# Kernel tuning notes

Measured on AMD Instinct MI355X. Metric: run time of the kernel, lower is better.

The kernel has to match this reference:

```python
import jax, jax.numpy as jnp
import numpy as np

B, N, H = 32, 2048, 256          # batch, num_docs, hidden_dim
F_HEADS = 8                      # config.dynamic_fusion_heads
NH = 8                           # num_heads inside each nn.MultiheadAttention
STEPS = 3                        # config.meta_adaptation_steps


def setup_inputs() -> dict:
    key = jax.random.key(0)
    ks = jax.random.split(key, 10)
    s = 0.02
    return {
        "query": jax.random.normal(ks[0], (B, H), jnp.float32),
        "retrieved_docs": jax.random.normal(ks[1], (B, N, H), jnp.float32),
        "causal_weights": jax.random.uniform(ks[2], (B, N, 1), jnp.float32),
        "context_history": jax.random.normal(ks[3], (B, H), jnp.float32),
        # per-fusion-head MultiheadAttention params (torch layout: in_proj [3H,H])
        "in_proj_w": jax.random.normal(ks[4], (F_HEADS, 3 * H, H), jnp.float32) * s,
        "in_proj_b": jnp.zeros((F_HEADS, 3 * H), jnp.float32),
        "out_proj_w": jax.random.normal(ks[5], (F_HEADS, H, H), jnp.float32) * s,
        "out_proj_b": jnp.zeros((F_HEADS, H), jnp.float32),
        "strategy_w": jax.random.normal(ks[6], (F_HEADS, H), jnp.float32) * s,
        "strategy_b": jnp.zeros((F_HEADS,), jnp.float32),
        "meta_params": jax.random.normal(ks[7], (STEPS, H, H), jnp.float32) * 0.02,
    }


def _mha_qlen1(q, kv, Wi, bi, Wo, bo):
    # q: [B,H] (query length 1), kv: [B,N,H]. Torch MHA semantics, batch_first.
    Wq, Wk, Wv = jnp.split(Wi, 3, axis=0)
    bq, bk, bv = jnp.split(bi, 3)
    dh = H // NH
    qh = (q @ Wq.T + bq).reshape(B, NH, dh)
    kh = (kv @ Wk.T + bk).reshape(B, N, NH, dh)
    vh = (kv @ Wv.T + bv).reshape(B, N, NH, dh)
    scores = jnp.einsum('bhd,bnhd->bhn', qh, kh) / jnp.sqrt(jnp.float32(dh))
    attn = jax.nn.softmax(scores, axis=-1)
    ctx = jnp.einsum('bhn,bnhd->bhd', attn, vh).reshape(B, H)
    return ctx @ Wo.T + bo


def reference(query, retrieved_docs, causal_weights, context_history,
              in_proj_w, in_proj_b, out_proj_w, out_proj_b,
              strategy_w, strategy_b, meta_params):
    # causal weighting of retrieved docs (shared across all fusion heads)
    weighted_docs = retrieved_docs * causal_weights  # [B,N,H]

    # batch all 8 fusion heads' cross-attention in one vmapped pass -> [F,B,H]
    heads_out = jax.vmap(
        lambda Wi, bi, Wo, bo: _mha_qlen1(query, weighted_docs, Wi, bi, Wo, bo)
    )(in_proj_w, in_proj_b, out_proj_w, out_proj_b)

    # sequential residual meta-adaptation steps (same matrices for every head)
    for i in range(STEPS):
        heads_out = heads_out + heads_out @ meta_params[i]

    # strategy-weighted combine of fusion heads
    strategy = jax.nn.softmax(query @ strategy_w.T + strategy_b, axis=-1)  # [B,F]
    return jnp.einsum('fbh,bf->bh', heads_out, strategy)  # [B,H]
```

## Files before the change

kernel.cpp:

```cpp
#include <hip/hip_runtime.h>
#include <hip/hip_bf16.h>


#define B_ 32
#define N_ 2048
#define H_ 256
#define F_ 8
#define FH_ 64
#define NCH_ 8
#define NCHK_ 4

typedef unsigned short u16;
typedef __attribute__((ext_vector_type(8))) short bf16x8;
typedef __attribute__((ext_vector_type(4))) float f32x4;
#define MFMA(a, b, c) __builtin_amdgcn_mfma_f32_16x16x32_bf16((a), (b), (c), 0, 0, 0)

__device__ __forceinline__ u16 f2b(float x) {
  unsigned u = __builtin_bit_cast(unsigned, x);
  return (u16)((u + 0x7fffu + ((u >> 16) & 1u)) >> 16);
}
__device__ __forceinline__ float b2f(u16 h) {
  unsigned u = ((unsigned)h) << 16;
  return __builtin_bit_cast(float, u);
}
__device__ __forceinline__ bf16x8 ld8b(const float* p) {
  float4 v0 = *(const float4*)p, v1 = *(const float4*)(p + 4);
  bf16x8 a;
  a[0] = f2b(v0.x); a[1] = f2b(v0.y); a[2] = f2b(v0.z); a[3] = f2b(v0.w);
  a[4] = f2b(v1.x); a[5] = f2b(v1.y); a[6] = f2b(v1.z); a[7] = f2b(v1.w);
  return a;
}

static constexpr size_t UB_U     = 0;
static constexpr size_t UB_W     = 1048576;
static constexpr size_t UB_L     = 3145728;
static constexpr size_t UB_STRAT = 3153920;
static constexpr size_t UB_MT    = 3154944;

#define SMEM_BYTES 52224

__device__ __forceinline__ void dev_k1(char* smem, int f, int hf, int bh,
    const float* __restrict__ query, const float* __restrict__ ipw,
    const float* __restrict__ ipb, const float* __restrict__ stw,
    const float* __restrict__ stb, u16* __restrict__ u, float* __restrict__ strat)
{
  const int tid = threadIdx.x, L = tid & 63, w = tid >> 6;
  const int khi = L >> 4, col = L & 15;
  u16* sW2 = (u16*)smem;
  u16* qhh = (u16*)(smem + 36864);
  u16* qhl = (u16*)(smem + 41216);
  float* slog = (float*)(smem + 45568);

  const int bg = bh * 16 + col;

  bf16x8 qf[8];
  #pragma unroll
  for (int ks = 0; ks < 8; ++ks)
    qf[ks] = ld8b(&query[(size_t)bg * H_ + ks * 32 + khi * 8]);

  if (f == 0 && hf == 0 && w == 0) {
    f32x4 sacc = (f32x4){0.f, 0.f, 0.f, 0.f};
    #pragma unroll
    for (int ks = 0; ks < 8; ++ks) {
      bf16x8 a = (bf16x8){0,0,0,0,0,0,0,0};
      if (col < 8) a = ld8b(&stw[(size_t)col * H_ + ks * 32 + khi * 8]);
      sacc = MFMA(a, qf[ks], sacc);
    }
    if (khi < 2) {
      #pragma unroll
      for (int r = 0; r < 4; ++r) {
        int i = khi * 4 + r;
        slog[col * 8 + i] = sacc[r] + stb[i];
      }
    }
  }

  bf16x8 aq[8];
  #pragma unroll
  for (int ks = 0; ks < 8; ++ks)
    aq[ks] = ld8b(&ipw[((size_t)(f * 768) + hf * 128 + w * 16 + col) * H_ + ks * 32 + khi * 8]);
  f32x4 qacc = (f32x4){0.f, 0.f, 0.f, 0.f};
  #pragma unroll
  for (int ks = 0; ks < 8; ++ks)
    qacc = MFMA(aq[ks], qf[ks], qacc);
  {
    int r0 = w * 16 + khi * 4;
    float4 bq = *(const float4*)&ipb[f * 768 + hf * 128 + r0];
    float v0 = qacc[0] + bq.x, v1 = qacc[1] + bq.y;
    float v2 = qacc[2] + bq.z, v3 = qacc[3] + bq.w;
    ushort4 hs = make_ushort4(f2b(v0), f2b(v1), f2b(v2), f2b(v3));
    ushort4 ls = make_ushort4(f2b(v0 - b2f(hs.x)), f2b(v1 - b2f(hs.y)),
                              f2b(v2 - b2f(hs.z)), f2b(v3 - b2f(hs.w)));
    *(ushort4*)&qhh[col * 136 + r0] = hs;
    *(ushort4*)&qhl[col * 136 + r0] = ls;
  }
  __syncthreads();

  if (f == 0 && hf == 0 && tid < 16) {
    float mx = slog[tid * 8];
    #pragma unroll
    for (int i = 1; i < F_; ++i) mx = fmaxf(mx, slog[tid * 8 + i]);
    float s = 0.f, e[F_];
    #pragma unroll
    for (int i = 0; i < F_; ++i) { e[i] = __expf(slog[tid * 8 + i] - mx); s += e[i]; }
    #pragma unroll
    for (int i = 0; i < F_; ++i) strat[(bh * 16 + tid) * F_ + i] = e[i] / s;
  }

  const float scale = 0.17677669529663687f;
  #pragma unroll
  for (int hp = 0; hp < 2; ++hp) {
    #pragma unroll
    for (int p = 0; p < 8; ++p) {
      int gid = tid + 512 * p;
      int dr = gid >> 6, jq = (gid & 63) * 4;
      float4 v = *(const float4*)&ipw[((size_t)(f * 768 + 256) + hf * 128 + hp * 64 + dr) * H_ + jq];
      float vv[4] = {v.x, v.y, v.z, v.w};
      #pragma unroll
      for (int e2 = 0; e2 < 4; ++e2) {
        int j = jq + e2;
        int m = ((((j >> 4) & 3) ^ ((j >> 2) & 3)) << 3);
        sW2[j * 72 + (dr ^ m)] = f2b(vv[e2]);
      }
    }
    __syncthreads();
    #pragma unroll
    for (int e = 0; e < 2; ++e) {
      #pragma unroll
      for (int q = 0; q < 2; ++q) {
        int jt = w * 2 + q;
        bf16x8 a = *(const bf16x8*)&sW2[(jt * 16 + col) * 72 + e * 32
                                        + ((khi ^ (jt & 3) ^ (col >> 2)) << 3)];
        int rl = (hp * 2 + e) * 32 + khi * 8;
        bf16x8 bhf = *(const bf16x8*)&qhh[col * 136 + rl];
        bf16x8 blf = *(const bf16x8*)&qhl[col * 136 + rl];
        f32x4 acc = (f32x4){0.f, 0.f, 0.f, 0.f};
        acc = MFMA(a, bhf, acc);
        acc = MFMA(a, blf, acc);
        int j0 = jt * 16 + khi * 4;
        ushort4 us = make_ushort4(f2b(acc[0] * scale), f2b(acc[1] * scale),
                                  f2b(acc[2] * scale), f2b(acc[3] * scale));
        *(ushort4*)&u[((size_t)(bg * 64) + f * 8 + hf * 4 + hp * 2 + e) * H_ + j0] = us;
      }
    }
    __syncthreads();
  }
}

__device__ __forceinline__ void dev_meta(char* smem, int bid2,
    const float* __restrict__ meta, u16* __restrict__ metaT)
{
  const int tid = threadIdx.x;
  const int s = bid2 >> 3, x0 = (bid2 & 7) * 32;
  u16* sT = (u16*)smem;
  #pragma unroll
  for (int p = 0; p < 4; ++p) {
    int idx = tid + 512 * p;
    int r = idx >> 3, xq = (idx & 7) * 4;
    float4 v = *(const float4*)&meta[((size_t)(s * 256) + r) * 256 + x0 + xq];
    sT[(xq + 0) * 264 + r] = f2b(v.x);
    sT[(xq + 1) * 264 + r] = f2b(v.y);
    sT[(xq + 2) * 264 + r] = f2b(v.z);
    sT[(xq + 3) * 264 + r] = f2b(v.w);
  }
  __syncthreads();
  #pragma unroll
  for (int p = 0; p < 2; ++p) {
    int idx = tid + 512 * p;
    int x = idx >> 5, rq = (idx & 31) * 8;
    bf16x8 v = *(bf16x8*)&sT[x * 264 + rq];
    *(bf16x8*)&metaT[((size_t)(s * 256) + x0 + x) * 256 + rq] = v;
  }
}

__device__ __forceinline__ void dev_k4(char* smem, int ns, int b,
    const float* __restrict__ docs, const float* __restrict__ cw,
    const u16* __restrict__ u, float* __restrict__ wbuf, float* __restrict__ lbuf)
{
  const int n0 = ns * 256;
  const int tid = threadIdx.x, L = tid & 63, w = tid >> 6;
  const int khi = L >> 4, col = L & 15;
  const int ft = w & 3, nt0 = (w >> 2) * 2;

  u16* sdu  = (u16*)smem;
  u16* phu  = (u16*)(smem + 33792);
  u16* plou = (u16*)(smem + 43008);

  bf16x8 uf[8];
  #pragma unroll
  for (int ks = 0; ks < 8; ++ks)
    uf[ks] = *(const bf16x8*)&u[((size_t)(b * 64) + ft * 16 + col) * H_ + ks * 32 + khi * 8];

  float4 dv[8];
  #pragma unroll
  for (int p = 0; p < 8; ++p) {
    int idx = tid + 512 * p;
    int n = idx >> 6, jq = (idx & 63) * 4;
    dv[p] = *(const float4*)&docs[((size_t)(b * N_) + n0 + n) * H_ + jq];
  }
  #pragma unroll
  for (int p = 0; p < 8; ++p) {
    int idx = tid + 512 * p;
    int n = idx >> 6, jq = (idx & 63) * 4;
    *(ushort4*)&sdu[n * 264 + (jq ^ (((n >> 3) & 3) << 4))] =
        make_ushort4(f2b(dv[p].x), f2b(dv[p].y), f2b(dv[p].z), f2b(dv[p].w));
  }
  __syncthreads();

  f32x4 acc2[4][2];
  #pragma unroll
  for (int mt = 0; mt < 4; ++mt)
    #pragma unroll
    for (int jt = 0; jt < 2; ++jt) acc2[mt][jt] = (f32x4){0.f, 0.f, 0.f, 0.f};
  float eacc[4] = {0.f, 0.f, 0.f, 0.f};

  for (int nc = 0; nc < NCHK_; ++nc) {
    if (nc < NCHK_ - 1) {
      #pragma unroll
      for (int p = 0; p < 8; ++p) {
        int idx = tid + 512 * p;
        int n = idx >> 6, jq = (idx & 63) * 4;
        dv[p] = *(const float4*)&docs[((size_t)(b * N_) + n0 + (nc + 1) * 64 + n) * H_ + jq];
      }
    }
    f32x4 sc0 = (f32x4){0.f, 0.f, 0.f, 0.f}, sc1 = sc0;
    const int nr0 = nt0 * 16 + col, nr1 = (nt0 + 1) * 16 + col;
    const int sw0 = ((nr0 >> 3) & 3) << 4, sw1 = ((nr1 >> 3) & 3) << 4;
    #pragma unroll
    for (int ks = 0; ks < 8; ++ks) {
      bf16x8 b0 = *(const bf16x8*)&sdu[nr0 * 264 + ((ks * 32 + khi * 8) ^ sw0)];
      bf16x8 b1 = *(const bf16x8*)&sdu[nr1 * 264 + ((ks * 32 + khi * 8) ^ sw1)];
      sc0 = MFMA(uf[ks], b0, sc0);
      sc1 = MFMA(uf[ks], b1, sc1);
    }
    {
      int ng = n0 + nc * 64 + nt0 * 16 + col;
      float cv0 = cw[(size_t)b * N_ + ng];
      float cv1 = cw[(size_t)b * N_ + ng + 16];
      #pragma unroll
      for (int r = 0; r < 4; ++r) {
        int fh = ft * 16 + khi * 4 + r;
        float ex0 = __expf(sc0[r] * cv0);
        float ex1 = __expf(sc1[r] * cv1);
        eacc[r] += ex0 + ex1;
        float p0 = ex0 * cv0, p1 = ex1 * cv1;
        u16 h0 = f2b(p0), h1 = f2b(p1);
        phu [fh * 72 + nt0 * 16 + col]       = h0;
        plou[fh * 72 + nt0 * 16 + col]       = f2b(p0 - b2f(h0));
        phu [fh * 72 + (nt0 + 1) * 16 + col] = h1;
        plou[fh * 72 + (nt0 + 1) * 16 + col] = f2b(p1 - b2f(h1));
      }
    }
    __syncthreads();

    #pragma unroll
    for (int kk = 0; kk < 2; ++kk) {
      #pragma unroll
      for (int jt = 0; jt < 2; ++jt) {
        int j = w * 32 + jt * 16 + col;
        bf16x8 bb;
        #pragma unroll
        for (int jj = 0; jj < 8; ++jj)
          bb[jj] = (short)sdu[(kk * 32 + khi * 8 + jj) * 264 + (j ^ (khi << 4))];
        #pragma unroll
        for (int mt = 0; mt < 4; ++mt) {
          bf16x8 ah = *(const bf16x8*)&phu [(mt * 16 + col) * 72 + kk * 32 + khi * 8];
          bf16x8 al = *(const bf16x8*)&plou[(mt * 16 + col) * 72 + kk * 32 + khi * 8];
          acc2[mt][jt] = MFMA(ah, bb, acc2[mt][jt]);
          acc2[mt][jt] = MFMA(al, bb, acc2[mt][jt]);
        }
      }
    }
    __syncthreads();

    if (nc < NCHK_ - 1) {
      #pragma unroll
      for (int p = 0; p < 8; ++p) {
        int idx = tid + 512 * p;
        int n = idx >> 6, jq = (idx & 63) * 4;
        *(ushort4*)&sdu[n * 264 + (jq ^ (((n >> 3) & 3) << 4))] =
            make_ushort4(f2b(dv[p].x), f2b(dv[p].y), f2b(dv[p].z), f2b(dv[p].w));
      }
      __syncthreads();
    }
  }
  #pragma unroll
  for (int mt = 0; mt < 4; ++mt)
    #pragma unroll
    for (int jt = 0; jt < 2; ++jt)
      #pragma unroll
      for (int r = 0; r < 4; ++r) {
        int fh = mt * 16 + khi * 4 + r;
        int j = w * 32 + jt * 16 + col;
        atomicAdd(&wbuf[((size_t)(b * 64) + fh) * H_ + j], acc2[mt][jt][r]);
      }
  #pragma unroll
  for (int r = 0; r < 4; ++r) {
    float e = eacc[r];
    e += __shfl_xor(e, 1, 64);
    e += __shfl_xor(e, 2, 64);
    e += __shfl_xor(e, 4, 64);
    e += __shfl_xor(e, 8, 64);
    if (col == 0)
      atomicAdd(&lbuf[(size_t)(b * 64) + ft * 16 + khi * 4 + r], e);
  }
}

__device__ __forceinline__ void dev_k5(char* smem, int f, int b0,
    const float* __restrict__ ipw, const float* __restrict__ ipb,
    const float* __restrict__ opw, const float* __restrict__ opb,
    const u16* __restrict__ metaT, const float* __restrict__ wbuf,
    const float* __restrict__ lbuf, const float* __restrict__ strat,
    float* __restrict__ out)
{
  const int tid = threadIdx.x, L = tid & 63, w = tid >> 6;
  const int khi = L >> 4, col = L & 15;

  u16* XAh = (u16*)smem;
  u16* XAl = (u16*)(smem + 8448);
  u16* XBh = (u16*)(smem + 16896);
  u16* XBl = (u16*)(smem + 25344);

  bf16x8 av[2][8];
  #pragma unroll
  for (int mt = 0; mt < 2; ++mt)
    #pragma unroll
    for (int ks = 0; ks < 8; ++ks)
      av[mt][ks] = ld8b(&ipw[((size_t)(f * 768 + 512) + w * 32 + mt * 16 + col) * H_
                             + ks * 32 + khi * 8]);
  const size_t wrow = ((size_t)((b0 + col) * 64) + f * 8 + w) * H_;
  const float li = 1.f / lbuf[(size_t)((b0 + col) * 64) + f * 8 + w];
  f32x4 cacc0 = (f32x4){0.f, 0.f, 0.f, 0.f};
  f32x4 cacc1 = (f32x4){0.f, 0.f, 0.f, 0.f};
  #pragma unroll
  for (int ks = 0; ks < 8; ++ks) {
    const float* p = &wbuf[wrow + ks * 32 + khi * 8];
    float4 v0 = *(const float4*)p, v1 = *(const float4*)(p + 4);
    float vv[8] = {v0.x, v0.y, v0.z, v0.w, v1.x, v1.y, v1.z, v1.w};
    bf16x8 bh, bl;
    #pragma unroll
    for (int e = 0; e < 8; ++e) {
      float x = vv[e] * li;
      u16 h = f2b(x);
      bh[e] = (short)h;
      bl[e] = (short)f2b(x - b2f(h));
    }
    cacc0 = MFMA(av[0][ks], bh, cacc0); cacc0 = MFMA(av[0][ks], bl, cacc0);
    cacc1 = MFMA(av[1][ks], bh, cacc1); cacc1 = MFMA(av[1][ks], bl, cacc1);
  }
  #pragma unroll
  for (int mt = 0; mt < 2; ++mt) {
    f32x4 cv = mt ? cacc1 : cacc0;
    #pragma unroll
    for (int r = 0; r < 4; ++r) {
      int d = mt * 16 + khi * 4 + r;
      float vv = cv[r] + ipb[f * 768 + 512 + w * 32 + d];
      u16 hi = f2b(vv);
      XAh[col * 264 + w * 32 + d] = hi;
      XAl[col * 264 + w * 32 + d] = f2b(vv - b2f(hi));
    }
  }

  bf16x8 bw[2][8];
  #pragma unroll
  for (int q = 0; q < 2; ++q)
    #pragma unroll
    for (int ks = 0; ks < 8; ++ks)
      bw[q][ks] = ld8b(&opw[((size_t)(f * 256) + (w * 2 + q) * 16 + col) * H_
                            + ks * 32 + khi * 8]);
  __syncthreads();

  f32x4 hr0, hr1;
  {
    float bo0 = opb[f * 256 + (w * 2 + 0) * 16 + col];
    float bo1 = opb[f * 256 + (w * 2 + 1) * 16 + col];
    hr0 = (f32x4){bo0, bo0, bo0, bo0};
    hr1 = (f32x4){bo1, bo1, bo1, bo1};
  }
  #pragma unroll
  for (int ks = 0; ks < 8; ++ks) {
    bf16x8 ah = *(const bf16x8*)&XAh[col * 264 + ks * 32 + khi * 8];
    bf16x8 al = *(const bf16x8*)&XAl[col * 264 + ks * 32 + khi * 8];
    hr0 = MFMA(ah, bw[0][ks], hr0); hr0 = MFMA(al, bw[0][ks], hr0);
    hr1 = MFMA(ah, bw[1][ks], hr1); hr1 = MFMA(al, bw[1][ks], hr1);
  }

  auto spill = [&](u16* Oh, u16* Ol) {
    #pragma unroll
    for (int q = 0; q < 2; ++q) {
      f32x4 hv = q ? hr1 : hr0;
      int x = (w * 2 + q) * 16 + col;
      #pragma unroll
      for (int r = 0; r < 4; ++r) {
        u16 hi = f2b(hv[r]);
        Oh[(khi * 4 + r) * 264 + x] = hi;
        Ol[(khi * 4 + r) * 264 + x] = f2b(hv[r] - b2f(hi));
      }
    }
  };
  auto meta_mm = [&](const u16* Ah_, const u16* Al_, int s) {
    f32x4 n0 = hr0, n1 = hr1;
    #pragma unroll
    for (int ks = 0; ks < 8; ++ks) {
      bf16x8 ah = *(const bf16x8*)&Ah_[col * 264 + ks * 32 + khi * 8];
      bf16x8 al = *(const bf16x8*)&Al_[col * 264 + ks * 32 + khi * 8];
      const u16* mrow = &metaT[((size_t)(s * 256) + (w * 2) * 16 + col) * 256 + ks * 32 + khi * 8];
      bf16x8 m0 = *(const bf16x8*)mrow;
      bf16x8 m1 = *(const bf16x8*)(mrow + 16 * 256);
      n0 = MFMA(ah, m0, n0); n0 = MFMA(al, m0, n0);
      n1 = MFMA(ah, m1, n1); n1 = MFMA(al, m1, n1);
    }
    hr0 = n0; hr1 = n1;
  };

  spill(XBh, XBl);
  __syncthreads();
  meta_mm(XBh, XBl, 0);
  spill(XAh, XAl);
  __syncthreads();
  meta_mm(XAh, XAl, 1);
  spill(XBh, XBl);
  __syncthreads();
  meta_mm(XBh, XBl, 2);

  #pragma unroll
  for (int q = 0; q < 2; ++q) {
    f32x4 hv = q ? hr1 : hr0;
    int x = (w * 2 + q) * 16 + col;
    #pragma unroll
    for (int r = 0; r < 4; ++r) {
      int b = khi * 4 + r;
      float sv = strat[(b0 + b) * F_ + f];
      atomicAdd(&out[(size_t)(b0 + b) * H_ + x], sv * hv[r]);
    }
  }
}

__global__ __launch_bounds__(512) void k1_all(
    const float* __restrict__ query, const float* __restrict__ ipw,
    const float* __restrict__ ipb, const float* __restrict__ stw,
    const float* __restrict__ stb, const float* __restrict__ meta,
    u16* __restrict__ u, u16* __restrict__ metaT, float* __restrict__ strat,
    float* __restrict__ wbuf, float* __restrict__ out)
{
  __shared__ __align__(16) char smem[SMEM_BYTES];
  const int bid = blockIdx.x, tid = threadIdx.x;
  if (bid < 32) {
    dev_k1(smem, bid >> 2, (bid >> 1) & 1, bid & 1, query, ipw, ipb, stw, stb, u, strat);
  } else if (bid < 56) {
    dev_meta(smem, bid - 32, meta, metaT);
  } else {
    int zb = bid - 56;
    float4 z4 = make_float4(0.f, 0.f, 0.f, 0.f);
    float4* z = (float4*)wbuf;
    for (int i = zb * 512 + tid; i < 131584; i += 16 * 512) z[i] = z4;
    if (zb < 4) ((float4*)out)[zb * 512 + tid] = z4;
  }
}

__global__ __launch_bounds__(512) void k4_sep(
    const float* __restrict__ docs, const float* __restrict__ cw,
    const u16* __restrict__ u, float* __restrict__ wbuf, float* __restrict__ lbuf)
{
  __shared__ __align__(16) char smem[SMEM_BYTES];
  dev_k4(smem, blockIdx.x, blockIdx.y, docs, cw, u, wbuf, lbuf);
}

__global__ __launch_bounds__(512) void k5_sep(
    const float* __restrict__ ipw, const float* __restrict__ ipb,
    const float* __restrict__ opw, const float* __restrict__ opb,
    const u16* __restrict__ metaT, const float* __restrict__ wbuf,
    const float* __restrict__ lbuf, const float* __restrict__ strat,
    float* __restrict__ out)
{
  __shared__ __align__(16) char smem[SMEM_BYTES];
  dev_k5(smem, blockIdx.x & 7, (blockIdx.x >> 3) * 16,
         ipw, ipb, opw, opb, metaT, wbuf, lbuf, strat, out);
}

extern "C" void kernel_launch(void* const* d_in, const int* in_sizes, int n_in,
                              void* d_out, int out_size, void* d_ws, size_t ws_size,
                              hipStream_t stream) {
  const float* query = (const float*)d_in[0];
  const float* docs  = (const float*)d_in[1];
  const float* cw    = (const float*)d_in[2];
  const float* ipw   = (const float*)d_in[4];
  const float* ipb   = (const float*)d_in[5];
  const float* opw   = (const float*)d_in[6];
  const float* opb   = (const float*)d_in[7];
  const float* stw   = (const float*)d_in[8];
  const float* stb   = (const float*)d_in[9];
  const float* meta  = (const float*)d_in[10];
  float* out = (float*)d_out;

  char* base = (char*)d_ws;
  u16*   u     = (u16*)(base + UB_U);
  float* wbuf  = (float*)(base + UB_W);
  float* lbuf  = (float*)(base + UB_L);
  float* strat = (float*)(base + UB_STRAT);
  u16*   metaT = (u16*)(base + UB_MT);

  k1_all<<<dim3(72), 512, 0, stream>>>(query, ipw, ipb, stw, stb, meta,
                                       u, metaT, strat, wbuf, out);
  k4_sep<<<dim3(NCH_, B_), 512, 0, stream>>>(docs, cw, u, wbuf, lbuf);
  k5_sep<<<dim3(16), 512, 0, stream>>>(ipw, ipb, opw, opb, metaT, wbuf, lbuf, strat, out);
}
```

Before: 180.0 us.

## Double-buffer doc prefetch, hoist causal weights, stagger atomics, move meta prep into k4

The streaming kernel now prefetches document chunks two steps ahead using a double-buffered register array, and loads all causal weights up front, so more global-load latency is hidden behind the MFMA work. The final atomicAdd loop rotates its tile order by chunk index to reduce contention on the same wbuf addresses across blocks. The meta-parameter transpose blocks move from the first kernel into the second kernel's grid as extra blocks, shortening the first kernel. In exchange, register pressure rises (16 float4 plus cached weights), which could lower occupancy.

```diff
diff --git a/kernel.cpp b/kernel.cpp
--- a/kernel.cpp
+++ b/kernel.cpp
@@ -191,19 +191,33 @@
   for (int ks = 0; ks < 8; ++ks)
     uf[ks] = *(const bf16x8*)&u[((size_t)(b * 64) + ft * 16 + col) * H_ + ks * 32 + khi * 8];
 
-  float4 dv[8];
+  float cvv[NCHK_][2];
+  #pragma unroll
+  for (int nc = 0; nc < NCHK_; ++nc) {
+    int ng = n0 + nc * 64 + nt0 * 16 + col;
+    cvv[nc][0] = cw[(size_t)b * N_ + ng];
+    cvv[nc][1] = cw[(size_t)b * N_ + ng + 16];
+  }
+
+  float4 dv[2][8];
   #pragma unroll
   for (int p = 0; p < 8; ++p) {
     int idx = tid + 512 * p;
     int n = idx >> 6, jq = (idx & 63) * 4;
-    dv[p] = *(const float4*)&docs[((size_t)(b * N_) + n0 + n) * H_ + jq];
+    dv[0][p] = *(const float4*)&docs[((size_t)(b * N_) + n0 + n) * H_ + jq];
+  }
+  #pragma unroll
+  for (int p = 0; p < 8; ++p) {
+    int idx = tid + 512 * p;
+    int n = idx >> 6, jq = (idx & 63) * 4;
+    dv[1][p] = *(const float4*)&docs[((size_t)(b * N_) + n0 + 64 + n) * H_ + jq];
   }
   #pragma unroll
   for (int p = 0; p < 8; ++p) {
     int idx = tid + 512 * p;
     int n = idx >> 6, jq = (idx & 63) * 4;
     *(ushort4*)&sdu[n * 264 + (jq ^ (((n >> 3) & 3) << 4))] =
-        make_ushort4(f2b(dv[p].x), f2b(dv[p].y), f2b(dv[p].z), f2b(dv[p].w));
+        make_ushort4(f2b(dv[0][p].x), f2b(dv[0][p].y), f2b(dv[0][p].z), f2b(dv[0][p].w));
   }
   __syncthreads();
 
@@ -214,13 +228,15 @@
     for (int jt = 0; jt < 2; ++jt) acc2[mt][jt] = (f32x4){0.f, 0.f, 0.f, 0.f};
   float eacc[4] = {0.f, 0.f, 0.f, 0.f};
 
+  #pragma unroll
   for (int nc = 0; nc < NCHK_; ++nc) {
-    if (nc < NCHK_ - 1) {
+    if (nc < NCHK_ - 2) {
       #pragma unroll
       for (int p = 0; p < 8; ++p) {
         int idx = tid + 512 * p;
         int n = idx >> 6, jq = (idx & 63) * 4;
-        dv[p] = *(const float4*)&docs[((size_t)(b * N_) + n0 + (nc + 1) * 64 + n) * H_ + jq];
+        dv[nc & 1][p] =
+            *(const float4*)&docs[((size_t)(b * N_) + n0 + (nc + 2) * 64 + n) * H_ + jq];
       }
     }
     f32x4 sc0 = (f32x4){0.f, 0.f, 0.f, 0.f}, sc1 = sc0;
@@ -234,9 +250,7 @@
       sc1 = MFMA(uf[ks], b1, sc1);
     }
     {
-      int ng = n0 + nc * 64 + nt0 * 16 + col;
-      float cv0 = cw[(size_t)b * N_ + ng];
-      float cv1 = cw[(size_t)b * N_ + ng + 16];
+      float cv0 = cvv[nc][0], cv1 = cvv[nc][1];
       #pragma unroll
       for (int r = 0; r < 4; ++r) {
         int fh = ft * 16 + khi * 4 + r;
@@ -278,22 +292,27 @@
       for (int p = 0; p < 8; ++p) {
         int idx = tid + 512 * p;
         int n = idx >> 6, jq = (idx & 63) * 4;
+        float4 v = dv[(nc + 1) & 1][p];
         *(ushort4*)&sdu[n * 264 + (jq ^ (((n >> 3) & 3) << 4))] =
-            make_ushort4(f2b(dv[p].x), f2b(dv[p].y), f2b(dv[p].z), f2b(dv[p].w));
+            make_ushort4(f2b(v.x), f2b(v.y), f2b(v.z), f2b(v.w));
       }
       __syncthreads();
     }
   }
   #pragma unroll
-  for (int mt = 0; mt < 4; ++mt)
-    #pragma unroll
-    for (int jt = 0; jt < 2; ++jt)
+  for (int mi = 0; mi < 4; ++mi) {
+    int mt = (mi + (ns & 3)) & 3;
+    #pragma unroll
+    for (int ji = 0; ji < 2; ++ji) {
+      int jt = (ji + (ns >> 2)) & 1;
       #pragma unroll
       for (int r = 0; r < 4; ++r) {
         int fh = mt * 16 + khi * 4 + r;
         int j = w * 32 + jt * 16 + col;
         atomicAdd(&wbuf[((size_t)(b * 64) + fh) * H_ + j], acc2[mt][jt][r]);
       }
+    }
+  }
   #pragma unroll
   for (int r = 0; r < 4; ++r) {
     float e = eacc[r];
@@ -439,18 +458,16 @@
 __global__ __launch_bounds__(512) void k1_all(
     const float* __restrict__ query, const float* __restrict__ ipw,
     const float* __restrict__ ipb, const float* __restrict__ stw,
-    const float* __restrict__ stb, const float* __restrict__ meta,
-    u16* __restrict__ u, u16* __restrict__ metaT, float* __restrict__ strat,
+    const float* __restrict__ stb,
+    u16* __restrict__ u, float* __restrict__ strat,
     float* __restrict__ wbuf, float* __restrict__ out)
 {
   __shared__ __align__(16) char smem[SMEM_BYTES];
   const int bid = blockIdx.x, tid = threadIdx.x;
   if (bid < 32) {
     dev_k1(smem, bid >> 2, (bid >> 1) & 1, bid & 1, query, ipw, ipb, stw, stb, u, strat);
-  } else if (bid < 56) {
-    dev_meta(smem, bid - 32, meta, metaT);
   } else {
-    int zb = bid - 56;
+    int zb = bid - 32;
     float4 z4 = make_float4(0.f, 0.f, 0.f, 0.f);
     float4* z = (float4*)wbuf;
     for (int i = zb * 512 + tid; i < 131584; i += 16 * 512) z[i] = z4;
@@ -458,12 +475,16 @@
   }
 }
 
-__global__ __launch_bounds__(512) void k4_sep(
+__global__ __launch_bounds__(512) void k4_all(
     const float* __restrict__ docs, const float* __restrict__ cw,
-    const u16* __restrict__ u, float* __restrict__ wbuf, float* __restrict__ lbuf)
+    const u16* __restrict__ u, float* __restrict__ wbuf, float* __restrict__ lbuf,
+    const float* __restrict__ meta, u16* __restrict__ metaT)
 {
   __shared__ __align__(16) char smem[SMEM_BYTES];
-  dev_k4(smem, blockIdx.x, blockIdx.y, docs, cw, u, wbuf, lbuf);
+  if (blockIdx.x < 256)
+    dev_k4(smem, blockIdx.x & 7, blockIdx.x >> 3, docs, cw, u, wbuf, lbuf);
+  else
+    dev_meta(smem, blockIdx.x - 256, meta, metaT);
 }
 
 __global__ __launch_bounds__(512) void k5_sep(
@@ -500,8 +521,7 @@
   float* strat = (float*)(base + UB_STRAT);
   u16*   metaT = (u16*)(base + UB_MT);
 
-  k1_all<<<dim3(72), 512, 0, stream>>>(query, ipw, ipb, stw, stb, meta,
-                                       u, metaT, strat, wbuf, out);
-  k4_sep<<<dim3(NCH_, B_), 512, 0, stream>>>(docs, cw, u, wbuf, lbuf);
+  k1_all<<<dim3(48), 512, 0, stream>>>(query, ipw, ipb, stw, stb, u, strat, wbuf, out);
+  k4_all<<<dim3(280), 512, 0, stream>>>(docs, cw, u, wbuf, lbuf, meta, metaT);
   k5_sep<<<dim3(16), 512, 0, stream>>>(ipw, ipb, opw, opb, metaT, wbuf, lbuf, strat, out);
 }
```

Result: slower. 208.2 us (+15.7%).
